# Kernel tuning notes

Hardware: AMD Instinct MI355X
Metric: run time of the kernel (lower is better)

Reference implementation:

```python
import jax, jax.numpy as jnp
import numpy as np

B, N, M, D = 8, 4096, 4096, 3

def setup_inputs() -> dict:
    key = jax.random.key(0)
    ks = jax.random.split(key, 6)
    return {
        "X_pred": jax.random.normal(ks[0], (B, N, D), dtype=jnp.float32),
        "X_true": jax.random.normal(ks[1], (B, M, D), dtype=jnp.float32),
        "R_pred": jax.random.normal(ks[2], (B, D, D), dtype=jnp.float32),
        "t_pred": jax.random.normal(ks[3], (B, D), dtype=jnp.float32),
        "R_true": jax.random.normal(ks[4], (B, D, D), dtype=jnp.float32),
        "t_true": jax.random.normal(ks[5], (B, D), dtype=jnp.float32),
        "temperature": jnp.asarray(0.1, dtype=jnp.float32),
    }

def reference(X_pred, X_true, R_pred, t_pred, R_true, t_true, temperature):
    # Rigid transforms: x' = R x + t
    Xp = jnp.einsum('bij,bnj->bni', R_pred, X_pred) + t_pred[:, None, :]  # (B,N,D)
    Xt = jnp.einsum('bij,bmj->bmi', R_true, X_true) + t_true[:, None, :]  # (B,M,D)
    # Squared pairwise distances: |a|^2 + |b|^2 - 2 a.b  (== cdist(p=2)**2)
    sq_p = jnp.sum(Xp * Xp, axis=-1)  # (B,N)
    sq_t = jnp.sum(Xt * Xt, axis=-1)  # (B,M)
    dist_sq = sq_p[:, :, None] + sq_t[:, None, :] - 2.0 * jnp.einsum('bnd,bmd->bnm', Xp, Xt)
    dist_sq = jnp.maximum(dist_sq, 0.0)  # (B,N,M)
    soft_alignment = jax.nn.softmax(-dist_sq / temperature, axis=-1)
    weighted_distances = jnp.sum(soft_alignment * dist_sq, axis=-1)  # (B,N)
    return jnp.mean(weighted_distances)
```

## Files before the change

### kernel.cpp

```cpp
#include <hip/hip_runtime.h>


#define B_    8
#define N_    4096
#define M_    4096
#define NWAVE 8
#define BLOCK (NWAVE * 64)
#define ROWS  256
#define MSPL  8
#define QCH   (M_ / MSPL)
#define WQ    (QCH / NWAVE)
#define LOG2E 1.4426950408889634f
#define LN2   0.6931471805599453f
#define BIGF  3.0e38f

__global__ __launch_bounds__(BLOCK, 8) void softfape_main(
    const float* __restrict__ X_pred, const float* __restrict__ X_true,
    const float* __restrict__ R_pred, const float* __restrict__ t_pred,
    const float* __restrict__ R_true, const float* __restrict__ t_true,
    const float* __restrict__ temp,
    float4* __restrict__ Pg)
{
    __shared__ float4 Q[QCH];
    __shared__ float  Mp[NWAVE][ROWS];
    __shared__ float  Lp[NWAVE][ROWS];
    __shared__ float  Sp[NWAVE][ROWS];
    __shared__ float  shl[ROWS];
    __shared__ float  pwl[ROWS];

    const int tid  = threadIdx.x;
    const int wave = tid >> 6;
    const int lane = tid & 63;
    const int x    = blockIdx.x;
    const int ms   = x & 7;
    const int rg   = (x >> 3) & 15;
    const int b    = x >> 7;

    const float T   = temp[0];
    const float c   = LOG2E / T;
    const float m2c = -2.0f * c;

    if (tid < QCH / 2) {
        const float g00 = R_true[b*9+0], g01 = R_true[b*9+1], g02 = R_true[b*9+2];
        const float g10 = R_true[b*9+3], g11 = R_true[b*9+4], g12 = R_true[b*9+5];
        const float g20 = R_true[b*9+6], g21 = R_true[b*9+7], g22 = R_true[b*9+8];
        const float u0  = t_true[b*3+0], u1 = t_true[b*3+1], u2 = t_true[b*3+2];
        const float2* xt = (const float2*)(X_true + ((size_t)b * M_ + ms * QCH) * 3);
        const float2 f0 = xt[3*tid+0], f1 = xt[3*tid+1], f2 = xt[3*tid+2];
        {
            const float y0 = fmaf(g00, f0.x, fmaf(g01, f0.y, fmaf(g02, f1.x, u0)));
            const float y1 = fmaf(g10, f0.x, fmaf(g11, f0.y, fmaf(g12, f1.x, u1)));
            const float y2 = fmaf(g20, f0.x, fmaf(g21, f0.y, fmaf(g22, f1.x, u2)));
            const float nn = fmaf(y0, y0, fmaf(y1, y1, y2 * y2));
            Q[2*tid]   = make_float4(m2c*y0, m2c*y1, m2c*y2, c*nn);
        }
        {
            const float y0 = fmaf(g00, f1.y, fmaf(g01, f2.x, fmaf(g02, f2.y, u0)));
            const float y1 = fmaf(g10, f1.y, fmaf(g11, f2.x, fmaf(g12, f2.y, u1)));
            const float y2 = fmaf(g20, f1.y, fmaf(g21, f2.x, fmaf(g22, f2.y, u2)));
            const float nn = fmaf(y0, y0, fmaf(y1, y1, y2 * y2));
            Q[2*tid+1] = make_float4(m2c*y0, m2c*y1, m2c*y2, c*nn);
        }
    }

    float px[4], py[4], pz[4], pw[4];
    {
        const float h00 = R_pred[b*9+0], h01 = R_pred[b*9+1], h02 = R_pred[b*9+2];
        const float h10 = R_pred[b*9+3], h11 = R_pred[b*9+4], h12 = R_pred[b*9+5];
        const float h20 = R_pred[b*9+6], h21 = R_pred[b*9+7], h22 = R_pred[b*9+8];
        const float v0 = t_pred[b*3+0], v1 = t_pred[b*3+1], v2 = t_pred[b*3+2];
        const float4* xp = (const float4*)(X_pred + ((size_t)b * N_ + rg * ROWS + lane * 4) * 3);
        const float4 a0 = xp[0], a1 = xp[1], a2 = xp[2];
        const float rx[4] = {a0.x, a0.w, a1.z, a2.y};
        const float ry[4] = {a0.y, a1.x, a1.w, a2.z};
        const float rz[4] = {a0.z, a1.y, a2.x, a2.w};
        #pragma unroll
        for (int r = 0; r < 4; ++r) {
            px[r] = fmaf(h00, rx[r], fmaf(h01, ry[r], fmaf(h02, rz[r], v0)));
            py[r] = fmaf(h10, rx[r], fmaf(h11, ry[r], fmaf(h12, rz[r], v1)));
            pz[r] = fmaf(h20, rx[r], fmaf(h21, ry[r], fmaf(h22, rz[r], v2)));
            pw[r] = c * fmaf(px[r], px[r], fmaf(py[r], py[r], pz[r] * pz[r]));
            pwl[4*lane + r] = pw[r];
        }
    }

    __syncthreads();

    const float4* __restrict__ Qw = Q + wave * WQ;

    float mA[4] = {BIGF, BIGF, BIGF, BIGF};
    #pragma unroll 8
    for (int k = 0; k < WQ; ++k) {
        const float4 q = Qw[k];
        #pragma unroll
        for (int r = 0; r < 4; ++r) {
            const float A = fmaf(q.x, px[r], fmaf(q.y, py[r], fmaf(q.z, pz[r], q.w)));
            mA[r] = fminf(mA[r], A);
        }
    }
    #pragma unroll
    for (int r = 0; r < 4; ++r) Mp[wave][4*lane + r] = mA[r];
    __syncthreads();

    if (tid < ROWS) {
        float m = Mp[0][tid];
        #pragma unroll
        for (int w2 = 1; w2 < NWAVE; ++w2) m = fminf(m, Mp[w2][tid]);
        shl[tid] = m;
    }
    __syncthreads();

    const float4 sh4 = *(const float4*)&shl[4*lane];
    const float sh[4] = {sh4.x, sh4.y, sh4.z, sh4.w};

    float L[4]  = {0.f, 0.f, 0.f, 0.f};
    float SA[4] = {0.f, 0.f, 0.f, 0.f};
    #pragma unroll 8
    for (int k = 0; k < WQ; ++k) {
        const float4 q = Qw[k];
        #pragma unroll
        for (int r = 0; r < 4; ++r) {
            const float A   = fmaf(q.x, px[r], fmaf(q.y, py[r], fmaf(q.z, pz[r], q.w)));
            const float arg = sh[r] - A;
            const float w   = __builtin_amdgcn_exp2f(arg);
            L[r] += w;
            SA[r] = fmaf(w, arg, SA[r]);
        }
    }
    #pragma unroll
    for (int r = 0; r < 4; ++r) {
        Lp[wave][4*lane + r] = L[r];
        Sp[wave][4*lane + r] = SA[r];
    }
    __syncthreads();

    if (tid < ROWS) {
        float Lr = 0.0f, Sr = 0.0f;
        #pragma unroll
        for (int w2 = 0; w2 < NWAVE; ++w2) { Lr += Lp[w2][tid]; Sr += Sp[w2][tid]; }
        const size_t row = (size_t)b * N_ + rg * ROWS + tid;
        Pg[row * MSPL + ms] = make_float4(shl[tid] + pwl[tid], Lr, Sr, 0.0f);
    }
}

__global__ __launch_bounds__(256) void softfape_finalize(
    const float4* __restrict__ Pg, const float* __restrict__ temp,
    float* __restrict__ out)
{
    __shared__ float ws4[4];
    const int tid = threadIdx.x;
    const size_t row = (size_t)blockIdx.x * 256 + tid;

    float4 P[MSPL];
    #pragma unroll
    for (int i = 0; i < MSPL; ++i) P[i] = Pg[row * MSPL + i];

    float m = P[0].x;
    #pragma unroll
    for (int i = 1; i < MSPL; ++i) m = fminf(m, P[i].x);

    float L = 0.0f, SA = 0.0f;
    #pragma unroll
    for (int i = 0; i < MSPL; ++i) {
        const float dm = m - P[i].x;
        const float f  = __builtin_amdgcn_exp2f(dm);
        L  = fmaf(P[i].y, f, L);
        SA = fmaf(f, fmaf(dm, P[i].y, P[i].z), SA);
    }
    float wd = m - SA / L;

    wd += __shfl_xor(wd, 1);  wd += __shfl_xor(wd, 2);  wd += __shfl_xor(wd, 4);
    wd += __shfl_xor(wd, 8);  wd += __shfl_xor(wd, 16); wd += __shfl_xor(wd, 32);
    if ((tid & 63) == 0) ws4[tid >> 6] = wd;
    __syncthreads();
    if (tid == 0) {
        const float s = ws4[0] + ws4[1] + ws4[2] + ws4[3];
        const float scale = temp[0] * LN2 / ((float)B_ * (float)N_);
        atomicAdd(out, s * scale);
    }
}

extern "C" void kernel_launch(void* const* d_in, const int* in_sizes, int n_in,
                              void* d_out, int out_size, void* d_ws, size_t ws_size,
                              hipStream_t stream) {
    const float* X_pred = (const float*)d_in[0];
    const float* X_true = (const float*)d_in[1];
    const float* R_pred = (const float*)d_in[2];
    const float* t_pred = (const float*)d_in[3];
    const float* R_true = (const float*)d_in[4];
    const float* t_true = (const float*)d_in[5];
    const float* temp   = (const float*)d_in[6];
    float* out = (float*)d_out;

    float4* Pg = (float4*)d_ws;

    hipMemsetAsync(out, 0, sizeof(float), stream);

    softfape_main<<<dim3(B_ * 16 * MSPL), BLOCK, 0, stream>>>(
        X_pred, X_true, R_pred, t_pred, R_true, t_true, temp, Pg);

    softfape_finalize<<<dim3((B_ * N_) / 256), 256, 0, stream>>>(Pg, temp, out);
}
```

Measured before the change: 101.9 us.

## Pack query points in SoA pairs and use packed fp32 FMA

Reorganizes the shared-memory query layout so two target points are stored interleaved (x pair, y pair, z pair, w pair) across two float4 slots. The distance computations in both passes then use 2-wide vector FMA/sub/add, which can map to packed fp32 instructions (v_pk_fma_f32) on CDNA, halving VALU instruction count for the non-exp math. Launch bounds drop from 8 to 4 blocks per CU, allowing more registers for the duplicated pred-point vectors at the cost of potential occupancy. The exp2 remains scalar, so it still bounds the second pass.

```diff
diff --git a/kernel.cpp b/kernel.cpp
--- a/kernel.cpp
+++ b/kernel.cpp
@@ -1,5 +1,8 @@
 #include <hip/hip_runtime.h>
 
+
+typedef float v2f __attribute__((ext_vector_type(2)));
+typedef float v4f __attribute__((ext_vector_type(4)));
 
 #define B_    8
 #define N_    4096
@@ -14,19 +17,19 @@
 #define LN2   0.6931471805599453f
 #define BIGF  3.0e38f
 
-__global__ __launch_bounds__(BLOCK, 8) void softfape_main(
+__global__ __launch_bounds__(BLOCK, 4) void softfape_main(
     const float* __restrict__ X_pred, const float* __restrict__ X_true,
     const float* __restrict__ R_pred, const float* __restrict__ t_pred,
     const float* __restrict__ R_true, const float* __restrict__ t_true,
     const float* __restrict__ temp,
     float4* __restrict__ Pg)
 {
-    __shared__ float4 Q[QCH];
-    __shared__ float  Mp[NWAVE][ROWS];
-    __shared__ float  Lp[NWAVE][ROWS];
-    __shared__ float  Sp[NWAVE][ROWS];
-    __shared__ float  shl[ROWS];
-    __shared__ float  pwl[ROWS];
+    __shared__ v4f   Q[QCH];
+    __shared__ float Mp[NWAVE][ROWS];
+    __shared__ float Lp[NWAVE][ROWS];
+    __shared__ float Sp[NWAVE][ROWS];
+    __shared__ float shl[ROWS];
+    __shared__ float pwl[ROWS];
 
     const int tid  = threadIdx.x;
     const int wave = tid >> 6;
@@ -47,23 +50,19 @@
         const float u0  = t_true[b*3+0], u1 = t_true[b*3+1], u2 = t_true[b*3+2];
         const float2* xt = (const float2*)(X_true + ((size_t)b * M_ + ms * QCH) * 3);
         const float2 f0 = xt[3*tid+0], f1 = xt[3*tid+1], f2 = xt[3*tid+2];
-        {
-            const float y0 = fmaf(g00, f0.x, fmaf(g01, f0.y, fmaf(g02, f1.x, u0)));
-            const float y1 = fmaf(g10, f0.x, fmaf(g11, f0.y, fmaf(g12, f1.x, u1)));
-            const float y2 = fmaf(g20, f0.x, fmaf(g21, f0.y, fmaf(g22, f1.x, u2)));
-            const float nn = fmaf(y0, y0, fmaf(y1, y1, y2 * y2));
-            Q[2*tid]   = make_float4(m2c*y0, m2c*y1, m2c*y2, c*nn);
-        }
-        {
-            const float y0 = fmaf(g00, f1.y, fmaf(g01, f2.x, fmaf(g02, f2.y, u0)));
-            const float y1 = fmaf(g10, f1.y, fmaf(g11, f2.x, fmaf(g12, f2.y, u1)));
-            const float y2 = fmaf(g20, f1.y, fmaf(g21, f2.x, fmaf(g22, f2.y, u2)));
-            const float nn = fmaf(y0, y0, fmaf(y1, y1, y2 * y2));
-            Q[2*tid+1] = make_float4(m2c*y0, m2c*y1, m2c*y2, c*nn);
-        }
-    }
-
-    float px[4], py[4], pz[4], pw[4];
+        const float a0 = fmaf(g00, f0.x, fmaf(g01, f0.y, fmaf(g02, f1.x, u0)));
+        const float a1 = fmaf(g10, f0.x, fmaf(g11, f0.y, fmaf(g12, f1.x, u1)));
+        const float a2 = fmaf(g20, f0.x, fmaf(g21, f0.y, fmaf(g22, f1.x, u2)));
+        const float an = fmaf(a0, a0, fmaf(a1, a1, a2 * a2));
+        const float b0 = fmaf(g00, f1.y, fmaf(g01, f2.x, fmaf(g02, f2.y, u0)));
+        const float b1 = fmaf(g10, f1.y, fmaf(g11, f2.x, fmaf(g12, f2.y, u1)));
+        const float b2 = fmaf(g20, f1.y, fmaf(g21, f2.x, fmaf(g22, f2.y, u2)));
+        const float bn = fmaf(b0, b0, fmaf(b1, b1, b2 * b2));
+        Q[2*tid]   = (v4f){m2c*a0, m2c*b0, m2c*a1, m2c*b1};
+        Q[2*tid+1] = (v4f){m2c*a2, m2c*b2, c*an,   c*bn  };
+    }
+
+    v2f Px[4], Py[4], Pz[4];
     {
         const float h00 = R_pred[b*9+0], h01 = R_pred[b*9+1], h02 = R_pred[b*9+2];
         const float h10 = R_pred[b*9+3], h11 = R_pred[b*9+4], h12 = R_pred[b*9+5];
@@ -76,26 +75,36 @@
         const float rz[4] = {a0.z, a1.y, a2.x, a2.w};
         #pragma unroll
         for (int r = 0; r < 4; ++r) {
-            px[r] = fmaf(h00, rx[r], fmaf(h01, ry[r], fmaf(h02, rz[r], v0)));
-            py[r] = fmaf(h10, rx[r], fmaf(h11, ry[r], fmaf(h12, rz[r], v1)));
-            pz[r] = fmaf(h20, rx[r], fmaf(h21, ry[r], fmaf(h22, rz[r], v2)));
-            pw[r] = c * fmaf(px[r], px[r], fmaf(py[r], py[r], pz[r] * pz[r]));
-            pwl[4*lane + r] = pw[r];
+            const float px = fmaf(h00, rx[r], fmaf(h01, ry[r], fmaf(h02, rz[r], v0)));
+            const float py = fmaf(h10, rx[r], fmaf(h11, ry[r], fmaf(h12, rz[r], v1)));
+            const float pz = fmaf(h20, rx[r], fmaf(h21, ry[r], fmaf(h22, rz[r], v2)));
+            const float pw = c * fmaf(px, px, fmaf(py, py, pz * pz));
+            pwl[4*lane + r] = pw;
+            Px[r] = (v2f){px, px};
+            Py[r] = (v2f){py, py};
+            Pz[r] = (v2f){pz, pz};
         }
     }
 
     __syncthreads();
 
-    const float4* __restrict__ Qw = Q + wave * WQ;
+    const v4f* __restrict__ Qw = Q + wave * WQ;
 
     float mA[4] = {BIGF, BIGF, BIGF, BIGF};
     #pragma unroll 8
-    for (int k = 0; k < WQ; ++k) {
-        const float4 q = Qw[k];
+    for (int k = 0; k < WQ/2; ++k) {
+        const v4f qa = Qw[2*k];
+        const v4f qb = Qw[2*k+1];
+        const v2f X2 = __builtin_shufflevector(qa, qa, 0, 1);
+        const v2f Y2 = __builtin_shufflevector(qa, qa, 2, 3);
+        const v2f Z2 = __builtin_shufflevector(qb, qb, 0, 1);
+        const v2f W2 = __builtin_shufflevector(qb, qb, 2, 3);
         #pragma unroll
         for (int r = 0; r < 4; ++r) {
-            const float A = fmaf(q.x, px[r], fmaf(q.y, py[r], fmaf(q.z, pz[r], q.w)));
-            mA[r] = fminf(mA[r], A);
+            const v2f A2 = __builtin_elementwise_fma(X2, Px[r],
+                           __builtin_elementwise_fma(Y2, Py[r],
+                           __builtin_elementwise_fma(Z2, Pz[r], W2)));
+            mA[r] = fminf(mA[r], fminf(A2.x, A2.y));
         }
     }
     #pragma unroll
@@ -111,26 +120,38 @@
     __syncthreads();
 
     const float4 sh4 = *(const float4*)&shl[4*lane];
-    const float sh[4] = {sh4.x, sh4.y, sh4.z, sh4.w};
-
-    float L[4]  = {0.f, 0.f, 0.f, 0.f};
-    float SA[4] = {0.f, 0.f, 0.f, 0.f};
+    const float shs[4] = {sh4.x, sh4.y, sh4.z, sh4.w};
+    v2f Sh[4];
+    #pragma unroll
+    for (int r = 0; r < 4; ++r) Sh[r] = (v2f){shs[r], shs[r]};
+
+    v2f L2[4], S2[4];
+    #pragma unroll
+    for (int r = 0; r < 4; ++r) { L2[r] = (v2f){0.f, 0.f}; S2[r] = (v2f){0.f, 0.f}; }
     #pragma unroll 8
-    for (int k = 0; k < WQ; ++k) {
-        const float4 q = Qw[k];
+    for (int k = 0; k < WQ/2; ++k) {
+        const v4f qa = Qw[2*k];
+        const v4f qb = Qw[2*k+1];
+        const v2f X2 = __builtin_shufflevector(qa, qa, 0, 1);
+        const v2f Y2 = __builtin_shufflevector(qa, qa, 2, 3);
+        const v2f Z2 = __builtin_shufflevector(qb, qb, 0, 1);
+        const v2f W2 = __builtin_shufflevector(qb, qb, 2, 3);
         #pragma unroll
         for (int r = 0; r < 4; ++r) {
-            const float A   = fmaf(q.x, px[r], fmaf(q.y, py[r], fmaf(q.z, pz[r], q.w)));
-            const float arg = sh[r] - A;
-            const float w   = __builtin_amdgcn_exp2f(arg);
-            L[r] += w;
-            SA[r] = fmaf(w, arg, SA[r]);
+            const v2f A2  = __builtin_elementwise_fma(X2, Px[r],
+                            __builtin_elementwise_fma(Y2, Py[r],
+                            __builtin_elementwise_fma(Z2, Pz[r], W2)));
+            const v2f arg = Sh[r] - A2;
+            const v2f w2  = {__builtin_amdgcn_exp2f(arg.x),
+                             __builtin_amdgcn_exp2f(arg.y)};
+            L2[r] += w2;
+            S2[r]  = __builtin_elementwise_fma(w2, arg, S2[r]);
         }
     }
     #pragma unroll
     for (int r = 0; r < 4; ++r) {
-        Lp[wave][4*lane + r] = L[r];
-        Sp[wave][4*lane + r] = SA[r];
+        Lp[wave][4*lane + r] = L2[r].x + L2[r].y;
+        Sp[wave][4*lane + r] = S2[r].x + S2[r].y;
     }
     __syncthreads();
 
```

Result: no change. 103.0 us (+1.1%).

## Replace two-pass min/exp with single-pass online softmax per row

Applied to the files above, without the earlier changes.

Switches from a two-pass scheme (first find the row minimum, then accumulate exp sums) to a single-pass online softmax. The running shift is only rescaled when the new value exceeds it by a threshold. Each thread now owns one row across the whole Q chunk instead of four rows over a per-wave slice, which removes the cross-wave shared-memory reductions and extra barriers. The cost is a data-dependent branch that can diverge within a wave, and every thread now reads all Q entries from LDS for a single row, so LDS traffic per unit of FMA work goes up.

```diff
diff --git a/kernel.cpp b/kernel.cpp
--- a/kernel.cpp
+++ b/kernel.cpp
@@ -5,16 +5,16 @@
 #define N_    4096
 #define M_    4096
 #define NWAVE 8
-#define BLOCK (NWAVE * 64)
-#define ROWS  256
+#define BLOCK 512
+#define RPB   512
 #define MSPL  8
 #define QCH   (M_ / MSPL)
-#define WQ    (QCH / NWAVE)
 #define LOG2E 1.4426950408889634f
 #define LN2   0.6931471805599453f
 #define BIGF  3.0e38f
+#define THR   8.0f
 
-__global__ __launch_bounds__(BLOCK, 8) void softfape_main(
+__global__ __launch_bounds__(BLOCK, 4) void softfape_main(
     const float* __restrict__ X_pred, const float* __restrict__ X_true,
     const float* __restrict__ R_pred, const float* __restrict__ t_pred,
     const float* __restrict__ R_true, const float* __restrict__ t_true,
@@ -22,19 +22,14 @@
     float4* __restrict__ Pg)
 {
     __shared__ float4 Q[QCH];
-    __shared__ float  Mp[NWAVE][ROWS];
-    __shared__ float  Lp[NWAVE][ROWS];
-    __shared__ float  Sp[NWAVE][ROWS];
-    __shared__ float  shl[ROWS];
-    __shared__ float  pwl[ROWS];
 
     const int tid  = threadIdx.x;
     const int wave = tid >> 6;
     const int lane = tid & 63;
     const int x    = blockIdx.x;
     const int ms   = x & 7;
-    const int rg   = (x >> 3) & 15;
-    const int b    = x >> 7;
+    const int rg   = (x >> 3) & 7;
+    const int b    = x >> 6;
 
     const float T   = temp[0];
     const float c   = LOG2E / T;
@@ -63,84 +58,49 @@
         }
     }
 
-    float px[4], py[4], pz[4], pw[4];
+    float px, py, pz, pw;
     {
         const float h00 = R_pred[b*9+0], h01 = R_pred[b*9+1], h02 = R_pred[b*9+2];
         const float h10 = R_pred[b*9+3], h11 = R_pred[b*9+4], h12 = R_pred[b*9+5];
         const float h20 = R_pred[b*9+6], h21 = R_pred[b*9+7], h22 = R_pred[b*9+8];
         const float v0 = t_pred[b*3+0], v1 = t_pred[b*3+1], v2 = t_pred[b*3+2];
-        const float4* xp = (const float4*)(X_pred + ((size_t)b * N_ + rg * ROWS + lane * 4) * 3);
-        const float4 a0 = xp[0], a1 = xp[1], a2 = xp[2];
-        const float rx[4] = {a0.x, a0.w, a1.z, a2.y};
-        const float ry[4] = {a0.y, a1.x, a1.w, a2.z};
-        const float rz[4] = {a0.z, a1.y, a2.x, a2.w};
-        #pragma unroll
-        for (int r = 0; r < 4; ++r) {
-            px[r] = fmaf(h00, rx[r], fmaf(h01, ry[r], fmaf(h02, rz[r], v0)));
-            py[r] = fmaf(h10, rx[r], fmaf(h11, ry[r], fmaf(h12, rz[r], v1)));
-            pz[r] = fmaf(h20, rx[r], fmaf(h21, ry[r], fmaf(h22, rz[r], v2)));
-            pw[r] = c * fmaf(px[r], px[r], fmaf(py[r], py[r], pz[r] * pz[r]));
-            pwl[4*lane + r] = pw[r];
-        }
+        const int row = rg * RPB + wave * 64 + lane;
+        const float* xp = X_pred + ((size_t)b * N_ + row) * 3;
+        const float rx = xp[0], ry = xp[1], rz = xp[2];
+        px = fmaf(h00, rx, fmaf(h01, ry, fmaf(h02, rz, v0)));
+        py = fmaf(h10, rx, fmaf(h11, ry, fmaf(h12, rz, v1)));
+        pz = fmaf(h20, rx, fmaf(h21, ry, fmaf(h22, rz, v2)));
+        pw = c * fmaf(px, px, fmaf(py, py, pz * pz));
     }
 
     __syncthreads();
 
-    const float4* __restrict__ Qw = Q + wave * WQ;
-
-    float mA[4] = {BIGF, BIGF, BIGF, BIGF};
-    #pragma unroll 8
-    for (int k = 0; k < WQ; ++k) {
-        const float4 q = Qw[k];
+    float s = BIGF, L = 0.0f, S = 0.0f;
+    for (int k0 = 0; k0 < QCH; k0 += 8) {
+        float4 qv[8];
         #pragma unroll
-        for (int r = 0; r < 4; ++r) {
-            const float A = fmaf(q.x, px[r], fmaf(q.y, py[r], fmaf(q.z, pz[r], q.w)));
-            mA[r] = fminf(mA[r], A);
+        for (int j = 0; j < 8; ++j) qv[j] = Q[k0 + j];
+        #pragma unroll
+        for (int j = 0; j < 8; ++j) {
+            const float4 q = qv[j];
+            const float A   = fmaf(q.x, px, fmaf(q.y, py, fmaf(q.z, pz, q.w)));
+            const float arg = s - A;
+            if (arg > THR) {
+                const float f = __builtin_amdgcn_exp2f(-arg);
+                S = f * fmaf(-arg, L, S);
+                L = fmaf(L, f, 1.0f);
+                s = A;
+            } else {
+                const float w = __builtin_amdgcn_exp2f(arg);
+                L += w;
+                S = fmaf(w, arg, S);
+            }
         }
     }
-    #pragma unroll
-    for (int r = 0; r < 4; ++r) Mp[wave][4*lane + r] = mA[r];
-    __syncthreads();
 
-    if (tid < ROWS) {
-        float m = Mp[0][tid];
-        #pragma unroll
-        for (int w2 = 1; w2 < NWAVE; ++w2) m = fminf(m, Mp[w2][tid]);
-        shl[tid] = m;
-    }
-    __syncthreads();
-
-    const float4 sh4 = *(const float4*)&shl[4*lane];
-    const float sh[4] = {sh4.x, sh4.y, sh4.z, sh4.w};
-
-    float L[4]  = {0.f, 0.f, 0.f, 0.f};
-    float SA[4] = {0.f, 0.f, 0.f, 0.f};
-    #pragma unroll 8
-    for (int k = 0; k < WQ; ++k) {
-        const float4 q = Qw[k];
-        #pragma unroll
-        for (int r = 0; r < 4; ++r) {
-            const float A   = fmaf(q.x, px[r], fmaf(q.y, py[r], fmaf(q.z, pz[r], q.w)));
-            const float arg = sh[r] - A;
-            const float w   = __builtin_amdgcn_exp2f(arg);
-            L[r] += w;
-            SA[r] = fmaf(w, arg, SA[r]);
-        }
-    }
-    #pragma unroll
-    for (int r = 0; r < 4; ++r) {
-        Lp[wave][4*lane + r] = L[r];
-        Sp[wave][4*lane + r] = SA[r];
-    }
-    __syncthreads();
-
-    if (tid < ROWS) {
-        float Lr = 0.0f, Sr = 0.0f;
-        #pragma unroll
-        for (int w2 = 0; w2 < NWAVE; ++w2) { Lr += Lp[w2][tid]; Sr += Sp[w2][tid]; }
-        const size_t row = (size_t)b * N_ + rg * ROWS + tid;
-        Pg[row * MSPL + ms] = make_float4(shl[tid] + pwl[tid], Lr, Sr, 0.0f);
-    }
+    const int row = rg * RPB + wave * 64 + lane;
+    const size_t grow = (size_t)b * N_ + row;
+    Pg[grow * MSPL + ms] = make_float4(s + pw, L, S, 0.0f);
 }
 
 __global__ __launch_bounds__(256) void softfape_finalize(
@@ -196,7 +156,7 @@
 
     hipMemsetAsync(out, 0, sizeof(float), stream);
 
-    softfape_main<<<dim3(B_ * 16 * MSPL), BLOCK, 0, stream>>>(
+    softfape_main<<<dim3(B_ * (N_ / RPB) * MSPL), BLOCK, 0, stream>>>(
         X_pred, X_true, R_pred, t_pred, R_true, t_true, temp, Pg);
 
     softfape_finalize<<<dim3((B_ * N_) / 256), 256, 0, stream>>>(Pg, temp, out);
```

Measured after the change: 119.3 us. +17.1%, slower.
